# Performance work log

Measured on AMD Instinct MI355X. Metric: run time of the kernel, lower is better.

Reference implementation:

```python
import jax, jax.numpy as jnp
import numpy as np

DIM = 128
HEADS = 4
HD = DIM // HEADS  # 32
WS = 8             # search window (ws x ws candidates)
K = 16             # top-k neighbors kept
SCALE = HD ** -0.5


def _sepconv(x, w_dw, w_pw, b):
    # depthwise 3x3 ('SAME', reflect-free) + pointwise 1x1 with bias (SepConv2d)
    C = x.shape[1]
    y = jax.lax.conv_general_dilated(x, w_dw, (1, 1), 'SAME',
                                     feature_group_count=C,
                                     dimension_numbers=('NCHW', 'OIHW', 'NCHW'))
    return jnp.einsum('bchw,oc->bohw', y, w_pw) + b[None, :, None, None]


def _refl(i, n):
    # dnls reflect_bounds: mirror indices back into [0, n-1]
    i = jnp.where(i < 0, -i, i)
    return jnp.where(i >= n, 2 * (n - 1) - i, i)


def _neighbor_idx(T, H, W, ws):
    # flat pixel index of the ws*ws spatial candidates per query (wt=0: same frame)
    off = jnp.arange(ws) - ws // 2
    ni = _refl(jnp.arange(H)[:, None] + off[None, :], H)  # [H,ws]
    nj = _refl(jnp.arange(W)[:, None] + off[None, :], W)  # [W,ws]
    pix = ni[:, None, :, None] * W + nj[None, :, None, :]  # [H,W,ws,ws]
    idx = jnp.arange(T)[:, None, None, None, None] * (H * W) + pix[None]
    return idx.reshape(T * H * W, ws * ws).astype(jnp.int32)  # [Q,L]


def reference(vid, wq_dw, wq_pw, bq, wk_dw, wk_pw, bk, wv_dw, wv_pw, bv, proj_w, proj_b):
    B, T, C, H, W = vid.shape
    Q = T * H * W
    x = vid.reshape(B * T, C, H, W)
    # qkv conv projection; q pre-scaled as in get_qkv
    q = _sepconv(x, wq_dw, wq_pw, bq) * SCALE
    k = _sepconv(x, wk_dw, wk_pw, bk)
    v = _sepconv(x, wv_dw, wv_pw, bv)

    def heads(z):  # [B*T,C,H,W] -> [B,heads,Q,hd]
        return z.reshape(B, T, HEADS, HD, H, W).transpose(0, 2, 1, 4, 5, 3).reshape(B, HEADS, Q, HD)

    qh, kh, vh = heads(q), heads(k), heads(v)
    idx = _neighbor_idx(T, H, W, WS)            # [Q,L]
    kg = jnp.take(kh, idx, axis=2)              # [B,h,Q,L,hd] irregular gather
    dists = jnp.einsum('bhqd,bhqld->bhql', qh, kg)
    vals, args = jax.lax.top_k(dists, K)        # k-NN by prod distance
    attn = jax.nn.softmax(vals, axis=-1)        # run_softmax over k
    sel = jnp.take_along_axis(jnp.broadcast_to(idx[None, None], (B, HEADS) + idx.shape), args, axis=-1)
    vsel = jnp.take_along_axis(vh, sel.reshape(B, HEADS, Q * K)[..., None], axis=2).reshape(B, HEADS, Q, K, HD)
    out = jnp.einsum('bhqk,bhqkd->bhqd', attn, vsel)   # wpsum (ps=pt=1)
    out = out.transpose(0, 2, 1, 3).reshape(B, Q, C)   # merge heads: (h c)
    y = out @ proj_w.T + proj_b                        # nn.Linear proj
    # fold: ps=1, stride0=1 -> zvid==1, pure reshape back to video
    return y.reshape(B, T, H, W, C).transpose(0, 1, 4, 2, 3)


def setup_inputs() -> dict:
    key = jax.random.key(0)
    ks = jax.random.split(key, 12)
    s = 0.02
    return {
        'vid': jax.random.normal(ks[0], (1, 2, DIM, 96, 96), jnp.float32),
        'wq_dw': jax.random.normal(ks[1], (DIM, 1, 3, 3), jnp.float32) * s,
        'wq_pw': jax.random.normal(ks[2], (DIM, DIM), jnp.float32) * s,
        'bq': jax.random.normal(ks[3], (DIM,), jnp.float32) * s,
        'wk_dw': jax.random.normal(ks[4], (DIM, 1, 3, 3), jnp.float32) * s,
        'wk_pw': jax.random.normal(ks[5], (DIM, DIM), jnp.float32) * s,
        'bk': jax.random.normal(ks[6], (DIM,), jnp.float32) * s,
        'wv_dw': jax.random.normal(ks[7], (DIM, 1, 3, 3), jnp.float32) * s,
        'wv_pw': jax.random.normal(ks[8], (DIM, DIM), jnp.float32) * s,
        'bv': jax.random.normal(ks[9], (DIM,), jnp.float32) * s,
        'proj_w': jax.random.normal(ks[10], (DIM, DIM), jnp.float32) * s,
        'proj_b': jax.random.normal(ks[11], (DIM,), jnp.float32) * s,
    }
```

## Files before the change

### kernel.cpp

```cpp
#include <hip/hip_runtime.h>
#include <math.h>

#define TT 2
#define CH 128
#define HH 96
#define WW 96
#define HWS 9216
#define QTOT 18432
#define QC (QTOT*CH)
#define HD 32
#define KTOP 16
#define SCALE 0.17677669529663687f

#define SEG 16
#define PR 8
#define PC 23
#define PSTRIDE 36

#define WB_TOT 98304

typedef __attribute__((ext_vector_type(8))) short short8;
typedef __attribute__((ext_vector_type(4))) float floatx4;

__device__ __forceinline__ unsigned short f2bf(float f) {
    union { float f; unsigned u; } x; x.f = f;
    unsigned r = x.u + 0x7fffu + ((x.u >> 16) & 1u);
    return (unsigned short)(r >> 16);
}
__device__ __forceinline__ float bf2f(unsigned short h) {
    return __uint_as_float(((unsigned)h) << 16);
}

__device__ __forceinline__ int refl(int x, int n) {
    x = x < 0 ? -x : x;
    return x >= n ? 2 * (n - 1) - x : x;
}

__global__ __launch_bounds__(256) void dwcvt_kernel(
    const float* __restrict__ x,
    const float* __restrict__ wq, const float* __restrict__ wk, const float* __restrict__ wv,
    const float* __restrict__ wq_pw, const float* __restrict__ wk_pw,
    const float* __restrict__ wv_pw, const float* __restrict__ proj_w,
    unsigned short* __restrict__ qk_hi,
    unsigned short* __restrict__ qk_lo,
    unsigned short* __restrict__ v_bf,
    unsigned short* __restrict__ wbuf)
{
    int t = threadIdx.x;
    if (blockIdx.x == 288) {
        int y = blockIdx.y;
        const float* src = y == 0 ? wq_pw : (y == 1 ? wk_pw : (y == 2 ? wv_pw : proj_w));
        unsigned short* hi = wbuf + (y == 0 ? 0 : (y == 1 ? 32768 : (y == 2 ? 65536 : 81920)));
#pragma unroll
        for (int r = 0; r < 16; r++) {
            int idx = r * 256 + t;
            float4 w4 = *(const float4*)(src + idx * 4);
            unsigned short hx = f2bf(w4.x), hy = f2bf(w4.y), hz = f2bf(w4.z), hw = f2bf(w4.w);
            uint2 pk;
            pk.x = hx | ((unsigned)hy << 16); pk.y = hz | ((unsigned)hw << 16);
            *(uint2*)(hi + idx * 4) = pk;
            if (y < 2) {
                unsigned short lx = f2bf(w4.x - bf2f(hx)), ly = f2bf(w4.y - bf2f(hy));
                unsigned short lz = f2bf(w4.z - bf2f(hz)), lw = f2bf(w4.w - bf2f(hw));
                pk.x = lx | ((unsigned)ly << 16); pk.y = lz | ((unsigned)lw << 16);
                *(uint2*)(hi + 16384 + idx * 4) = pk;
            }
        }
        return;
    }

    int pl = t & 63;
    int cg = __builtin_amdgcn_readfirstlane(t >> 6);
    int p  = blockIdx.x * 64 + pl;
    int c0 = blockIdx.y * 32 + cg * 8;
    int hw = p % HWS;
    int tt = p / HWS;
    int i = hw / WW, j = hw % WW;

    unsigned qh[4], ql[4], kh[4], kl[4], vh4[4];
#pragma unroll
    for (int ic = 0; ic < 8; ic += 2) {
        float sv[3][2];
#pragma unroll
        for (int u = 0; u < 2; u++) {
            int c = c0 + ic + u;
            const float* xp = x + (size_t)(tt * CH + c) * HWS;
            float w0[9], w1[9], w2[9];
#pragma unroll
            for (int r = 0; r < 9; r++) {
                w0[r] = wq[c * 9 + r]; w1[r] = wk[c * 9 + r]; w2[r] = wv[c * 9 + r];
            }
            float s0 = 0.f, s1 = 0.f, s2 = 0.f;
#pragma unroll
            for (int r = 0; r < 3; r++) {
                int ii = i + r - 1;
                if (ii < 0 || ii >= HH) continue;
#pragma unroll
                for (int ss = 0; ss < 3; ss++) {
                    int jj = j + ss - 1;
                    if (jj < 0 || jj >= WW) continue;
                    float xv = xp[ii * WW + jj];
                    s0 += xv * w0[r * 3 + ss];
                    s1 += xv * w1[r * 3 + ss];
                    s2 += xv * w2[r * 3 + ss];
                }
            }
            sv[0][u] = s0; sv[1][u] = s1; sv[2][u] = s2;
        }
        int w = ic >> 1;
        unsigned short h0 = f2bf(sv[0][0]), h1 = f2bf(sv[0][1]);
        qh[w] = h0 | ((unsigned)h1 << 16);
        ql[w] = f2bf(sv[0][0] - bf2f(h0)) | ((unsigned)f2bf(sv[0][1] - bf2f(h1)) << 16);
        h0 = f2bf(sv[1][0]); h1 = f2bf(sv[1][1]);
        kh[w] = h0 | ((unsigned)h1 << 16);
        kl[w] = f2bf(sv[1][0] - bf2f(h0)) | ((unsigned)f2bf(sv[1][1] - bf2f(h1)) << 16);
        vh4[w] = f2bf(sv[2][0]) | ((unsigned)f2bf(sv[2][1]) << 16);
    }
    size_t off = (size_t)p * CH + c0;
    uint4 pk;
    pk.x = qh[0]; pk.y = qh[1]; pk.z = qh[2]; pk.w = qh[3];
    *(uint4*)(qk_hi + off) = pk;
    pk.x = ql[0]; pk.y = ql[1]; pk.z = ql[2]; pk.w = ql[3];
    *(uint4*)(qk_lo + off) = pk;
    pk.x = kh[0]; pk.y = kh[1]; pk.z = kh[2]; pk.w = kh[3];
    *(uint4*)(qk_hi + (size_t)QC + off) = pk;
    pk.x = kl[0]; pk.y = kl[1]; pk.z = kl[2]; pk.w = kl[3];
    *(uint4*)(qk_lo + (size_t)QC + off) = pk;
    pk.x = vh4[0]; pk.y = vh4[1]; pk.z = vh4[2]; pk.w = vh4[3];
    *(uint4*)(v_bf + off) = pk;
}

__global__ __launch_bounds__(256) void qkv_mfma(
    const unsigned short* __restrict__ Ahi,
    const unsigned short* __restrict__ Alo,
    const unsigned short* __restrict__ Avb,
    const unsigned short* __restrict__ wbuf,
    const float* __restrict__ bq, const float* __restrict__ bk, const float* __restrict__ bv,
    float* __restrict__ qkf,
    unsigned short* __restrict__ vh)
{
    __shared__ unsigned short WhS[128 * 136];
    __shared__ unsigned short WlS[128 * 136];
    int sel = blockIdx.y;
    int t = threadIdx.x;
    int wv = t >> 6, lane = t & 63;
    int m = lane & 15, quad = lane >> 4;
    int p0 = blockIdx.x * 64;
    int o0 = wv * 32;

    if (sel == 2) {
        const unsigned short* Wg = wbuf + 65536;
#pragma unroll
        for (int r = 0; r < 16; r++) {
            int lin = r * 256 + t;
            int o = lin >> 5, cq = lin & 31;
            *(uint2*)(&WhS[o * 136 + cq * 4]) = *(const uint2*)(Wg + o * CH + cq * 4);
        }
        __syncthreads();
        float bb[2];
#pragma unroll
        for (int ot = 0; ot < 2; ot++) bb[ot] = bv[o0 + ot * 16 + m];
        floatx4 acc[4][2];
#pragma unroll
        for (int i = 0; i < 4; i++)
#pragma unroll
            for (int j = 0; j < 2; j++) acc[i][j] = (floatx4){0.f, 0.f, 0.f, 0.f};
#pragma unroll
        for (int kc = 0; kc < 4; kc++) {
            short8 a[4], b[2];
#pragma unroll
            for (int pt = 0; pt < 4; pt++)
                a[pt] = *(const short8*)(Avb + (size_t)(p0 + pt * 16 + m) * CH + kc * 32 + quad * 8);
#pragma unroll
            for (int ot = 0; ot < 2; ot++)
                b[ot] = *(const short8*)(&WhS[(o0 + ot * 16 + m) * 136 + kc * 32 + quad * 8]);
#pragma unroll
            for (int pt = 0; pt < 4; pt++)
#pragma unroll
                for (int ot = 0; ot < 2; ot++)
                    acc[pt][ot] = __builtin_amdgcn_mfma_f32_16x16x32_bf16(a[pt], b[ot], acc[pt][ot], 0, 0, 0);
        }
        unsigned short* vhh = vh + (size_t)wv * QTOT * 32;
#pragma unroll
        for (int pt = 0; pt < 4; pt++)
#pragma unroll
            for (int ot = 0; ot < 2; ot++)
#pragma unroll
                for (int reg = 0; reg < 4; reg++) {
                    int p = p0 + pt * 16 + quad * 4 + reg;
                    vhh[(size_t)p * 32 + ot * 16 + m] = f2bf(acc[pt][ot][reg] + bb[ot]);
                }
        return;
    }

    const unsigned short* Wh_g = wbuf + sel * 32768;
    const unsigned short* Wl_g = Wh_g + 16384;
    const float* bias = sel ? bk : bq;
    float scale = sel ? 1.f : SCALE;
    const unsigned short* ah = Ahi + (size_t)sel * QC;
    const unsigned short* al = Alo + (size_t)sel * QC;
    float* O = qkf + (size_t)sel * QC;

#pragma unroll
    for (int r = 0; r < 16; r++) {
        int lin = r * 256 + t;
        int o = lin >> 5, cq = lin & 31;
        *(uint2*)(&WhS[o * 136 + cq * 4]) = *(const uint2*)(Wh_g + o * CH + cq * 4);
        *(uint2*)(&WlS[o * 136 + cq * 4]) = *(const uint2*)(Wl_g + o * CH + cq * 4);
    }
    __syncthreads();
    float bb[2];
#pragma unroll
    for (int ot = 0; ot < 2; ot++) bb[ot] = bias[o0 + ot * 16 + m];
    floatx4 acc[4][2];
#pragma unroll
    for (int i = 0; i < 4; i++)
#pragma unroll
        for (int j = 0; j < 2; j++) acc[i][j] = (floatx4){0.f, 0.f, 0.f, 0.f};
#pragma unroll
    for (int kc = 0; kc < 4; kc++) {
        short8 avh[4], avl[4], bh[2], bl[2];
#pragma unroll
        for (int pt = 0; pt < 4; pt++) {
            size_t base = (size_t)(p0 + pt * 16 + m) * CH + kc * 32 + quad * 8;
            avh[pt] = *(const short8*)(ah + base);
            avl[pt] = *(const short8*)(al + base);
        }
#pragma unroll
        for (int ot = 0; ot < 2; ot++) {
            int lidx = (o0 + ot * 16 + m) * 136 + kc * 32 + quad * 8;
            bh[ot] = *(const short8*)(&WhS[lidx]);
            bl[ot] = *(const short8*)(&WlS[lidx]);
        }
#pragma unroll
        for (int pt = 0; pt < 4; pt++)
#pragma unroll
            for (int ot = 0; ot < 2; ot++) {
                acc[pt][ot] = __builtin_amdgcn_mfma_f32_16x16x32_bf16(avh[pt], bh[ot], acc[pt][ot], 0, 0, 0);
                acc[pt][ot] = __builtin_amdgcn_mfma_f32_16x16x32_bf16(avh[pt], bl[ot], acc[pt][ot], 0, 0, 0);
                acc[pt][ot] = __builtin_amdgcn_mfma_f32_16x16x32_bf16(avl[pt], bh[ot], acc[pt][ot], 0, 0, 0);
            }
    }
#pragma unroll
    for (int pt = 0; pt < 4; pt++)
#pragma unroll
        for (int ot = 0; ot < 2; ot++)
#pragma unroll
            for (int reg = 0; reg < 4; reg++) {
                int p = p0 + pt * 16 + quad * 4 + reg;
                O[(size_t)p * CH + o0 + ot * 16 + m] = (acc[pt][ot][reg] + bb[ot]) * scale;
            }
}

__global__ __launch_bounds__(256) void attn_kernel(
    const float* __restrict__ q,
    const float* __restrict__ k,
    const unsigned short* __restrict__ vh,
    unsigned short* __restrict__ att)
{
    __shared__ float kp[PR * PC * PSTRIDE];
    __shared__ uint2 slot[4][16];
    int h = blockIdx.y;
    int n = blockIdx.x;
    int seg = (n & 7) * 144 + (n >> 3);
    int qj0 = (seg % (WW / SEG)) * SEG;
    int qi = (seg / (WW / SEG)) % HH;
    int tt = seg / ((WW / SEG) * HH);
    int t = threadIdx.x;

#pragma unroll
    for (int r = 0; r < 6; r++) {
        int f = r * 256 + t;
        if (f < PR * PC * 8) {
            int pix = f >> 3, d4 = f & 7;
            int ci = pix / PC, cj = pix - ci * PC;
            int gi = refl(qi + ci - 4, HH);
            int gj = refl(qj0 + cj - 4, WW);
            int gp = tt * HWS + gi * WW + gj;
            *(float4*)(&kp[pix * PSTRIDE + d4 * 4]) =
                *(const float4*)(k + (size_t)gp * CH + h * HD + d4 * 4);
        }
    }

    int wv = t >> 6, lane = t & 63;
    if (lane < KTOP) slot[wv][lane] = make_uint2(0u, 0u);
    __syncthreads();

    int ci = lane >> 3, cjo = lane & 7;
    int di = ci - 4, dj = cjo - 4;
    int rowoff = tt * HWS + refl(qi + di, HH) * WW;
    const int d = lane & (HD - 1);
    const unsigned long long below = (1ull << lane) - 1ull;
    const unsigned short* vhh = vh + (size_t)h * QTOT * 32;

    for (int ql = wv * 4; ql < wv * 4 + 4; ql++) {
        int qj = qj0 + ql;
        int p = tt * HWS + qi * WW + qj;
        const float* qp = q + (size_t)p * CH + h * HD;
        const float* kr = &kp[(ci * PC + ql + cjo) * PSTRIDE];
        float dist = 0.f;
#pragma unroll
        for (int dd = 0; dd < 8; dd++) {
            float4 qv = *(const float4*)(qp + dd * 4);
            float4 kv = *(const float4*)(kr + dd * 4);
            dist += qv.x * kv.x + qv.y * kv.y + qv.z * kv.z + qv.w * kv.w;
        }
        int cpix = rowoff + refl(qj + dj, WW);

        unsigned u = __float_as_uint(dist);
        unsigned key = (u & 0x80000000u) ? ~u : (u | 0x80000000u);

        unsigned prefix = 0u;
        int need = KTOP;
#pragma unroll
        for (int bit = 31; bit >= 0; --bit) {
            unsigned hi = (prefix >> bit) | 1u;
            unsigned long long b = __ballot((key >> bit) == hi);
            int cnt = __popcll(b);
            bool take = cnt >= need;
            prefix = take ? (prefix | (1u << bit)) : prefix;
            need = take ? need : need - cnt;
        }
        bool isEq = (key == prefix);
        unsigned long long eqm = __ballot(isEq);
        int rk = __popcll(eqm & below);
        bool selb = (key > prefix) || (isEq && rk < need);
        unsigned long long selm = __ballot(selb);

        float e = selb ? __expf(dist) : 0.f;

        int rksel = __builtin_amdgcn_mbcnt_hi(
            (unsigned)(selm >> 32), __builtin_amdgcn_mbcnt_lo((unsigned)selm, 0));
        if (selb && rksel < KTOP) slot[wv][rksel] = make_uint2(__float_as_uint(e), (unsigned)cpix);

        float acc = 0.f, denom = 0.f;
#pragma unroll
        for (int r = 0; r < KTOP; r++) {
            uint2 sp = slot[wv][r];
            float a0 = __uint_as_float(sp.x);
            denom += a0;
            acc += a0 * bf2f(vhh[(size_t)sp.y * 32 + d]);
        }
        if (lane < HD)
            att[(size_t)p * CH + h * HD + lane] = f2bf(acc / denom);
    }
}

__global__ __launch_bounds__(256) void proj_mfma(
    const unsigned short* __restrict__ A,
    const unsigned short* __restrict__ wbuf,
    const float* __restrict__ bias,
    float* __restrict__ out)
{
    __shared__ unsigned short Ws[128 * 136];
    const unsigned short* Wg = wbuf + 81920;
    int t = threadIdx.x;
#pragma unroll
    for (int r = 0; r < 16; r++) {
        int lin = r * 256 + t;
        int o = lin >> 5, cq = lin & 31;
        *(uint2*)(&Ws[o * 136 + cq * 4]) = *(const uint2*)(Wg + o * CH + cq * 4);
    }
    __syncthreads();
    int wv = t >> 6, lane = t & 63;
    int m = lane & 15, quad = lane >> 4;
    int p0 = blockIdx.x * 64;
    int o0 = wv * 32;
    float bb[2][4];
#pragma unroll
    for (int ot = 0; ot < 2; ot++)
#pragma unroll
        for (int reg = 0; reg < 4; reg++) bb[ot][reg] = bias[o0 + ot * 16 + quad * 4 + reg];
    floatx4 acc[2][4];
#pragma unroll
    for (int i = 0; i < 2; i++)
#pragma unroll
        for (int j = 0; j < 4; j++) acc[i][j] = (floatx4){0.f, 0.f, 0.f, 0.f};
#pragma unroll
    for (int kc = 0; kc < 4; kc++) {
        short8 a[2], b[4];
#pragma unroll
        for (int ot = 0; ot < 2; ot++)
            a[ot] = *(const short8*)(&Ws[(o0 + ot * 16 + m) * 136 + kc * 32 + quad * 8]);
#pragma unroll
        for (int pt = 0; pt < 4; pt++)
            b[pt] = *(const short8*)(A + (size_t)(p0 + pt * 16 + m) * CH + kc * 32 + quad * 8);
#pragma unroll
        for (int ot = 0; ot < 2; ot++)
#pragma unroll
            for (int pt = 0; pt < 4; pt++)
                acc[ot][pt] = __builtin_amdgcn_mfma_f32_16x16x32_bf16(a[ot], b[pt], acc[ot][pt], 0, 0, 0);
    }
    int tt = p0 / HWS;
    int hwb = p0 - tt * HWS;
#pragma unroll
    for (int ot = 0; ot < 2; ot++)
#pragma unroll
        for (int pt = 0; pt < 4; pt++)
#pragma unroll
            for (int reg = 0; reg < 4; reg++) {
                int o = o0 + ot * 16 + quad * 4 + reg;
                int hw = hwb + pt * 16 + m;
                out[((size_t)(tt * CH + o)) * HWS + hw] = acc[ot][pt][reg] + bb[ot][reg];
            }
}

extern "C" void kernel_launch(void* const* d_in, const int* in_sizes, int n_in,
                              void* d_out, int out_size, void* d_ws, size_t ws_size,
                              hipStream_t stream) {
    const float* vid    = (const float*)d_in[0];
    const float* wq_dw  = (const float*)d_in[1];
    const float* wq_pw  = (const float*)d_in[2];
    const float* bq     = (const float*)d_in[3];
    const float* wk_dw  = (const float*)d_in[4];
    const float* wk_pw  = (const float*)d_in[5];
    const float* bk     = (const float*)d_in[6];
    const float* wv_dw  = (const float*)d_in[7];
    const float* wv_pw  = (const float*)d_in[8];
    const float* bv     = (const float*)d_in[9];
    const float* proj_w = (const float*)d_in[10];
    const float* proj_b = (const float*)d_in[11];
    float* out = (float*)d_out;

    float* qkf = (float*)d_ws;
    unsigned short* vh = (unsigned short*)(qkf + (size_t)2 * QC);
    unsigned short* qk_hi = vh + (size_t)QC;
    unsigned short* qk_lo = qk_hi + (size_t)2 * QC;
    unsigned short* v_bf = qk_lo + (size_t)2 * QC;
    unsigned short* wbuf = v_bf + (size_t)QC;
    unsigned short* att_bf = v_bf;

    dwcvt_kernel<<<dim3(289, 4), 256, 0, stream>>>(
        vid, wq_dw, wk_dw, wv_dw, wq_pw, wk_pw, wv_pw, proj_w,
        qk_hi, qk_lo, v_bf, wbuf);
    qkv_mfma<<<dim3(QTOT / 64, 3), 256, 0, stream>>>(
        qk_hi, qk_lo, v_bf, wbuf, bq, bk, bv, qkf, vh);
    attn_kernel<<<dim3(TT * HH * (WW / SEG), 4), 256, 0, stream>>>(
        qkf, qkf + (size_t)QC, vh, att_bf);
    proj_mfma<<<QTOT / 64, 256, 0, stream>>>(att_bf, wbuf, proj_b, out);
}
```

Measured before the change: 194.0 us.

## Interleave four queries per wave in top-k radix select and split V gather

Each wave now computes distances for its four queries up front, then runs the 32-bit radix threshold search for all four together so the ballots of independent queries can overlap. The select loop is simplified to a single >= comparison per bit, with the tie count worked out afterwards. The V accumulation splits the 16 neighbors across the two 32-lane halves and combines them with a shuffle, using a fast reciprocal in place of the division. In exchange, register use rises and the shared slot array grows four times.

Result: faster. 185.8 us (-4.2%).

```diff
diff --git a/kernel.cpp b/kernel.cpp
--- a/kernel.cpp
+++ b/kernel.cpp
@@ -259,7 +259,7 @@
     unsigned short* __restrict__ att)
 {
     __shared__ float kp[PR * PC * PSTRIDE];
-    __shared__ uint2 slot[4][16];
+    __shared__ uint2 slot[4][4][16];
     int h = blockIdx.y;
     int n = blockIdx.x;
     int seg = (n & 7) * 144 + (n >> 3);
@@ -283,66 +283,87 @@
     }
 
     int wv = t >> 6, lane = t & 63;
-    if (lane < KTOP) slot[wv][lane] = make_uint2(0u, 0u);
+    slot[wv][lane >> 4][lane & 15] = make_uint2(0u, 0u);
     __syncthreads();
 
     int ci = lane >> 3, cjo = lane & 7;
     int di = ci - 4, dj = cjo - 4;
     int rowoff = tt * HWS + refl(qi + di, HH) * WW;
-    const int d = lane & (HD - 1);
     const unsigned long long below = (1ull << lane) - 1ull;
     const unsigned short* vhh = vh + (size_t)h * QTOT * 32;
 
-    for (int ql = wv * 4; ql < wv * 4 + 4; ql++) {
-        int qj = qj0 + ql;
-        int p = tt * HWS + qi * WW + qj;
-        const float* qp = q + (size_t)p * CH + h * HD;
+    float dist[4];
+#pragma unroll
+    for (int qq = 0; qq < 4; qq++) {
+        int ql = wv * 4 + qq;
+        const float* qp = q + (size_t)(tt * HWS + qi * WW + qj0 + ql) * CH + h * HD;
         const float* kr = &kp[(ci * PC + ql + cjo) * PSTRIDE];
-        float dist = 0.f;
+        float s = 0.f;
 #pragma unroll
         for (int dd = 0; dd < 8; dd++) {
             float4 qv = *(const float4*)(qp + dd * 4);
             float4 kv = *(const float4*)(kr + dd * 4);
-            dist += qv.x * kv.x + qv.y * kv.y + qv.z * kv.z + qv.w * kv.w;
-        }
-        int cpix = rowoff + refl(qj + dj, WW);
-
-        unsigned u = __float_as_uint(dist);
-        unsigned key = (u & 0x80000000u) ? ~u : (u | 0x80000000u);
-
-        unsigned prefix = 0u;
-        int need = KTOP;
-#pragma unroll
-        for (int bit = 31; bit >= 0; --bit) {
-            unsigned hi = (prefix >> bit) | 1u;
-            unsigned long long b = __ballot((key >> bit) == hi);
-            int cnt = __popcll(b);
-            bool take = cnt >= need;
-            prefix = take ? (prefix | (1u << bit)) : prefix;
-            need = take ? need : need - cnt;
-        }
-        bool isEq = (key == prefix);
-        unsigned long long eqm = __ballot(isEq);
+            s += qv.x * kv.x + qv.y * kv.y + qv.z * kv.z + qv.w * kv.w;
+        }
+        dist[qq] = s;
+    }
+
+    unsigned key[4], L[4];
+#pragma unroll
+    for (int qq = 0; qq < 4; qq++) {
+        unsigned u = __float_as_uint(dist[qq]);
+        key[qq] = (u & 0x80000000u) ? ~u : (u | 0x80000000u);
+        L[qq] = 0u;
+    }
+#pragma unroll
+    for (int bit = 31; bit >= 0; --bit) {
+#pragma unroll
+        for (int qq = 0; qq < 4; qq++) {
+            unsigned C = L[qq] | (1u << bit);
+            unsigned long long b = __ballot(key[qq] >= C);
+            L[qq] = (__popcll(b) >= KTOP) ? C : L[qq];
+        }
+    }
+
+#pragma unroll
+    for (int qq = 0; qq < 4; qq++) {
+        unsigned T = L[qq];
+        bool gt = key[qq] > T;
+        unsigned long long gtm = __ballot(gt);
+        int need = KTOP - __popcll(gtm);
+        bool eq = key[qq] == T;
+        unsigned long long eqm = __ballot(eq);
         int rk = __popcll(eqm & below);
-        bool selb = (key > prefix) || (isEq && rk < need);
+        bool selb = gt || (eq && rk < need);
         unsigned long long selm = __ballot(selb);
-
-        float e = selb ? __expf(dist) : 0.f;
-
+        float e = selb ? __expf(dist[qq]) : 0.f;
         int rksel = __builtin_amdgcn_mbcnt_hi(
             (unsigned)(selm >> 32), __builtin_amdgcn_mbcnt_lo((unsigned)selm, 0));
-        if (selb && rksel < KTOP) slot[wv][rksel] = make_uint2(__float_as_uint(e), (unsigned)cpix);
-
+        int qj = qj0 + wv * 4 + qq;
+        int cpix = rowoff + refl(qj + dj, WW);
+        if (selb && rksel < KTOP)
+            slot[wv][qq][rksel] = make_uint2(__float_as_uint(e), (unsigned)cpix);
+    }
+
+    const int d = lane & (HD - 1);
+    const int half8 = (lane >> 5) * 8;
+#pragma unroll
+    for (int qq = 0; qq < 4; qq++) {
         float acc = 0.f, denom = 0.f;
 #pragma unroll
-        for (int r = 0; r < KTOP; r++) {
-            uint2 sp = slot[wv][r];
+        for (int r = 0; r < 8; r++) {
+            uint2 sp = slot[wv][qq][half8 + r];
             float a0 = __uint_as_float(sp.x);
             denom += a0;
             acc += a0 * bf2f(vhh[(size_t)sp.y * 32 + d]);
         }
-        if (lane < HD)
-            att[(size_t)p * CH + h * HD + lane] = f2bf(acc / denom);
+        acc += __shfl_xor(acc, 32);
+        denom += __shfl_xor(denom, 32);
+        if (lane < HD) {
+            int p = tt * HWS + qi * WW + qj0 + wv * 4 + qq;
+            att[(size_t)p * CH + h * HD + lane] =
+                f2bf(acc * __builtin_amdgcn_rcpf(denom));
+        }
     }
 }
 
```

## Widen attention block to one wave per query with swizzled K patch and split gather

Applied to the files above, without the earlier changes.

The attention kernel grows from 256 to 1024 threads so each of 16 waves handles one query column, replacing the per-wave 4-query loop. The K patch in shared memory is XOR-swizzled to cut bank conflicts, and the top-k radix select is simplified to a threshold search on key >= candidate. The V gather is split across the two wave halves (8 slots each) and combined with a shuffle, with a reciprocal replacing the divide. This adds parallelism and shortens the per-wave serial chain, at the cost of larger blocks, which may reduce scheduling flexibility and occupancy.

New measurement: 182.8 us. -5.8%, faster.

```diff
diff --git a/kernel.cpp b/kernel.cpp
--- a/kernel.cpp
+++ b/kernel.cpp
@@ -252,14 +252,14 @@
             }
 }
 
-__global__ __launch_bounds__(256) void attn_kernel(
+__global__ __launch_bounds__(1024) void attn_kernel(
     const float* __restrict__ q,
     const float* __restrict__ k,
     const unsigned short* __restrict__ vh,
     unsigned short* __restrict__ att)
 {
     __shared__ float kp[PR * PC * PSTRIDE];
-    __shared__ uint2 slot[4][16];
+    __shared__ uint2 slot[16][KTOP];
     int h = blockIdx.y;
     int n = blockIdx.x;
     int seg = (n & 7) * 144 + (n >> 3);
@@ -269,81 +269,87 @@
     int t = threadIdx.x;
 
 #pragma unroll
-    for (int r = 0; r < 6; r++) {
-        int f = r * 256 + t;
+    for (int r = 0; r < 2; r++) {
+        int f = r * 1024 + t;
         if (f < PR * PC * 8) {
             int pix = f >> 3, d4 = f & 7;
             int ci = pix / PC, cj = pix - ci * PC;
             int gi = refl(qi + ci - 4, HH);
             int gj = refl(qj0 + cj - 4, WW);
             int gp = tt * HWS + gi * WW + gj;
-            *(float4*)(&kp[pix * PSTRIDE + d4 * 4]) =
+            int sw = (pix >> 3) & 7;
+            *(float4*)(&kp[pix * PSTRIDE + ((d4 ^ sw) << 2)]) =
                 *(const float4*)(k + (size_t)gp * CH + h * HD + d4 * 4);
         }
     }
 
     int wv = t >> 6, lane = t & 63;
-    if (lane < KTOP) slot[wv][lane] = make_uint2(0u, 0u);
+    int wvu = __builtin_amdgcn_readfirstlane(wv);
+    if (lane < KTOP) slot[wvu][lane] = make_uint2(0u, 0u);
     __syncthreads();
 
     int ci = lane >> 3, cjo = lane & 7;
     int di = ci - 4, dj = cjo - 4;
     int rowoff = tt * HWS + refl(qi + di, HH) * WW;
-    const int d = lane & (HD - 1);
     const unsigned long long below = (1ull << lane) - 1ull;
     const unsigned short* vhh = vh + (size_t)h * QTOT * 32;
 
-    for (int ql = wv * 4; ql < wv * 4 + 4; ql++) {
-        int qj = qj0 + ql;
-        int p = tt * HWS + qi * WW + qj;
-        const float* qp = q + (size_t)p * CH + h * HD;
-        const float* kr = &kp[(ci * PC + ql + cjo) * PSTRIDE];
-        float dist = 0.f;
-#pragma unroll
-        for (int dd = 0; dd < 8; dd++) {
-            float4 qv = *(const float4*)(qp + dd * 4);
-            float4 kv = *(const float4*)(kr + dd * 4);
-            dist += qv.x * kv.x + qv.y * kv.y + qv.z * kv.z + qv.w * kv.w;
-        }
-        int cpix = rowoff + refl(qj + dj, WW);
-
-        unsigned u = __float_as_uint(dist);
-        unsigned key = (u & 0x80000000u) ? ~u : (u | 0x80000000u);
-
-        unsigned prefix = 0u;
-        int need = KTOP;
-#pragma unroll
-        for (int bit = 31; bit >= 0; --bit) {
-            unsigned hi = (prefix >> bit) | 1u;
-            unsigned long long b = __ballot((key >> bit) == hi);
-            int cnt = __popcll(b);
-            bool take = cnt >= need;
-            prefix = take ? (prefix | (1u << bit)) : prefix;
-            need = take ? need : need - cnt;
-        }
-        bool isEq = (key == prefix);
-        unsigned long long eqm = __ballot(isEq);
-        int rk = __popcll(eqm & below);
-        bool selb = (key > prefix) || (isEq && rk < need);
-        unsigned long long selm = __ballot(selb);
-
-        float e = selb ? __expf(dist) : 0.f;
-
-        int rksel = __builtin_amdgcn_mbcnt_hi(
-            (unsigned)(selm >> 32), __builtin_amdgcn_mbcnt_lo((unsigned)selm, 0));
-        if (selb && rksel < KTOP) slot[wv][rksel] = make_uint2(__float_as_uint(e), (unsigned)cpix);
-
-        float acc = 0.f, denom = 0.f;
-#pragma unroll
-        for (int r = 0; r < KTOP; r++) {
-            uint2 sp = slot[wv][r];
-            float a0 = __uint_as_float(sp.x);
-            denom += a0;
-            acc += a0 * bf2f(vhh[(size_t)sp.y * 32 + d]);
-        }
-        if (lane < HD)
-            att[(size_t)p * CH + h * HD + lane] = f2bf(acc / denom);
-    }
+    int ql = wvu;
+    int qj = qj0 + ql;
+    int p = tt * HWS + qi * WW + qj;
+
+    const float* qp = q + (size_t)p * CH + h * HD;
+    int pixq = ci * PC + ql + cjo;
+    const float* kr = &kp[pixq * PSTRIDE];
+    int sq = (pixq >> 3) & 7;
+    float dist = 0.f;
+#pragma unroll
+    for (int dd = 0; dd < 8; dd++) {
+        float4 qv = *(const float4*)(qp + dd * 4);
+        float4 kv = *(const float4*)(kr + ((dd ^ sq) << 2));
+        dist += qv.x * kv.x + qv.y * kv.y + qv.z * kv.z + qv.w * kv.w;
+    }
+
+    unsigned u = __float_as_uint(dist);
+    unsigned key = (u & 0x80000000u) ? ~u : (u | 0x80000000u);
+    unsigned L = 0u;
+#pragma unroll
+    for (int bit = 31; bit >= 0; --bit) {
+        unsigned C = L | (1u << bit);
+        unsigned long long b = __ballot(key >= C);
+        L = (__popcll(b) >= KTOP) ? C : L;
+    }
+
+    bool gt = key > L;
+    unsigned long long gtm = __ballot(gt);
+    int need = KTOP - __popcll(gtm);
+    bool eq = (key == L);
+    unsigned long long eqm = __ballot(eq);
+    int rk = __popcll(eqm & below);
+    bool selb = gt || (eq && rk < need);
+    unsigned long long selm = __ballot(selb);
+    float e = selb ? __expf(dist) : 0.f;
+    int rksel = __builtin_amdgcn_mbcnt_hi(
+        (unsigned)(selm >> 32), __builtin_amdgcn_mbcnt_lo((unsigned)selm, 0));
+    int cpix = rowoff + refl(qj + dj, WW);
+    if (selb && rksel < KTOP)
+        slot[wvu][rksel] = make_uint2(__float_as_uint(e), (unsigned)(cpix << 5));
+
+    const int d = lane & (HD - 1);
+    const int half8 = (lane >> 5) * 8;
+    float acc = 0.f, denom = 0.f;
+#pragma unroll
+    for (int r = 0; r < 8; r++) {
+        uint2 sp = slot[wvu][half8 + r];
+        float a0 = __uint_as_float(sp.x);
+        denom += a0;
+        acc += a0 * bf2f(vhh[(size_t)sp.y + d]);
+    }
+    acc += __shfl_xor(acc, 32);
+    denom += __shfl_xor(denom, 32);
+    if (lane < HD)
+        att[(size_t)p * CH + h * HD + lane] =
+            f2bf(acc * __builtin_amdgcn_rcpf(denom));
 }
 
 __global__ __launch_bounds__(256) void proj_mfma(
@@ -435,7 +441,7 @@
         qk_hi, qk_lo, v_bf, wbuf);
     qkv_mfma<<<dim3(QTOT / 64, 3), 256, 0, stream>>>(
         qk_hi, qk_lo, v_bf, wbuf, bq, bk, bv, qkf, vh);
-    attn_kernel<<<dim3(TT * HH * (WW / SEG), 4), 256, 0, stream>>>(
+    attn_kernel<<<dim3(TT * HH * (WW / SEG), 4), 1024, 0, stream>>>(
         qkf, qkf + (size_t)QC, vh, att_bf);
     proj_mfma<<<QTOT / 64, 256, 0, stream>>>(att_bf, wbuf, proj_b, out);
 }
```
